# Optimization experiments

Measured on AMD Instinct MI355X. Metric: run time of the kernel, lower is better.

The kernel has to match this reference:

```python
import jax, jax.numpy as jnp
import numpy as np

FEATURE_DIM = 1024
HEAD_NUM = 16
HIDDEN_DIM = FEATURE_DIM // HEAD_NUM


def setup_inputs() -> dict:
    key = jax.random.key(0)
    ks = jax.random.split(key, 12)
    B, S, D = 4, 2048, FEATURE_DIM
    s = 1.0 / np.sqrt(D)
    inp = {
        "query": jax.random.normal(ks[0], (B, S, D), jnp.float32),
        "key": jax.random.normal(ks[1], (B, S, D), jnp.float32),
        "value": jax.random.normal(ks[2], (B, S, D), jnp.float32),
        "mask": jax.random.randint(ks[3], (B, 1, 1, S), 0, 2, jnp.int32),
        "Wq": jax.random.normal(ks[4], (D, D), jnp.float32) * s,
        "bq": jnp.zeros((D,), jnp.float32),
        "Wk": jax.random.normal(ks[5], (D, D), jnp.float32) * s,
        "bk": jnp.zeros((D,), jnp.float32),
        "Wv": jax.random.normal(ks[6], (D, D), jnp.float32) * s,
        "bv": jnp.zeros((D,), jnp.float32),
        "Wo": jax.random.normal(ks[7], (D, D), jnp.float32) * s,
        "bo": jnp.zeros((D,), jnp.float32),
    }
    return inp


def reference(query, key, value, mask, Wq, bq, Wk, bk, Wv, bv, Wo, bo):
    B, Sq, D = query.shape
    H, Hd = HEAD_NUM, HIDDEN_DIM
    scale = jnp.sqrt(jnp.asarray(Hd, query.dtype))

    def split_heads(x):
        b, s, _ = x.shape
        return x.reshape(b, s, H, Hd).transpose(0, 2, 1, 3)  # [B,H,S,Hd]

    Q = split_heads(query @ Wq.T + bq)
    K = split_heads(key @ Wk.T + bk)
    V = split_heads(value @ Wv.T + bv)

    scores = jnp.einsum("bhqd,bhkd->bhqk", Q, K) / scale
    scores = jnp.where(mask == 0, jnp.asarray(-1e10, scores.dtype), scores)
    attn = jax.nn.softmax(scores, axis=-1)  # dropout p=0 -> identity
    h = jnp.einsum("bhqk,bhkd->bhqd", attn, V)
    h = h.transpose(0, 2, 1, 3).reshape(B, Sq, D)
    return h @ Wo.T + bo
```

## Files before the change

### kernel.cpp

```cpp
#include <hip/hip_runtime.h>
#include <hip/hip_bf16.h>
#include <cstdint>
#include <cstddef>

#define D_MODEL 1024
#define SEQ     2048
#define BATCH   4
#define NHEAD   16
#define HD      64
#define MROWS   (BATCH * SEQ)

typedef __attribute__((ext_vector_type(8))) short  short8;
typedef __attribute__((ext_vector_type(4))) float  floatx4;
typedef __attribute__((ext_vector_type(4))) unsigned short ushort4v;
typedef unsigned short u16;

__device__ __forceinline__ u16 f2bf(float x) {
    __hip_bfloat16 h = __float2bfloat16(x);
    return *(u16*)&h;
}

__device__ __forceinline__ void async_copy16(const u16* g, u16* l) {
    __builtin_amdgcn_global_load_lds(
        (const __attribute__((address_space(1))) void*)g,
        (__attribute__((address_space(3))) void*)l, 16, 0, 0);
}

__device__ __forceinline__ void cvt8(const float* s, u16* d, size_t i) {
    const float4 a = *(const float4*)(s + i);
    const float4 b = *(const float4*)(s + i + 4);
    short8 o;
    o[0] = (short)f2bf(a.x); o[1] = (short)f2bf(a.y);
    o[2] = (short)f2bf(a.z); o[3] = (short)f2bf(a.w);
    o[4] = (short)f2bf(b.x); o[5] = (short)f2bf(b.y);
    o[6] = (short)f2bf(b.z); o[7] = (short)f2bf(b.w);
    *(short8*)(d + i) = o;
}

__global__ __launch_bounds__(256) void cvt4(
    const float* __restrict__ s0, const float* __restrict__ s1,
    const float* __restrict__ s2, const float* __restrict__ s3,
    u16* __restrict__ d0, u16* __restrict__ d1,
    u16* __restrict__ d2, u16* __restrict__ d3)
{
    const float* s = blockIdx.y == 0 ? s0 : (blockIdx.y == 1 ? s1 :
                     (blockIdx.y == 2 ? s2 : s3));
    u16*         d = blockIdx.y == 0 ? d0 : (blockIdx.y == 1 ? d1 :
                     (blockIdx.y == 2 ? d2 : d3));
    cvt8(s, d, ((size_t)blockIdx.x * 256 + threadIdx.x) * 8);
}

__global__ __launch_bounds__(256) void gemm_qkv(
    const float* __restrict__ Aq, const float* __restrict__ Ak,
    const float* __restrict__ Av,
    const u16* __restrict__ Wqp, const u16* __restrict__ Wkp,
    const u16* __restrict__ Wvp,
    const float* __restrict__ bqp, const float* __restrict__ bkp,
    const float* __restrict__ bvp,
    u16* __restrict__ oq, u16* __restrict__ ok, u16* __restrict__ ov)
{
    constexpr int K = D_MODEL;
    __shared__ __align__(16) u16 smem[16384];
    u16 (*As)[64] = (u16(*)[64])smem;
    u16 (*Ws)[64] = (u16(*)[64])(smem + 8192);

    const int z = blockIdx.z;
    const float* A    = z == 0 ? Aq  : (z == 1 ? Ak  : Av);
    const u16*   W    = z == 0 ? Wqp : (z == 1 ? Wkp : Wvp);
    const float* bias = z == 0 ? bqp : (z == 1 ? bkp : bvp);
    u16*         out  = z == 0 ? oq  : (z == 1 ? ok  : ov);

    const int bm = blockIdx.x * 128;
    const int bn = blockIdx.y * 128;
    const int t  = threadIdx.x;
    const int w  = t >> 6;
    const int l  = t & 63;
    const int li = l & 15;
    const int quad = l >> 4;
    const int wm = (w & 1) * 64;
    const int wn = (w >> 1) * 64;
    const int srow = w * 32 + (l >> 3);
    const int lc8  = (l & 7) * 8;

    const float* Ab = A + (size_t)bm * K;
    const u16*   Wb = W + (size_t)bn * K;

    float4 pa[4][2];
    short8 pw[4];
    #pragma unroll
    for (int j = 0; j < 4; j++) {
        const float* ap = Ab + (size_t)(srow + j * 8) * K + lc8;
        pa[j][0] = *(const float4*)ap;
        pa[j][1] = *(const float4*)(ap + 4);
        pw[j] = *(const short8*)(Wb + (size_t)(srow + j * 8) * K + lc8);
    }

    floatx4 acc[4][4];
    #pragma unroll
    for (int mi = 0; mi < 4; mi++)
        #pragma unroll
        for (int ni = 0; ni < 4; ni++) acc[mi][ni] = (floatx4){0.f,0.f,0.f,0.f};

    for (int kt = 0; kt < K; kt += 64) {
        __syncthreads();
        #pragma unroll
        for (int j = 0; j < 4; j++) {
            short8 av;
            av[0] = (short)f2bf(pa[j][0].x); av[1] = (short)f2bf(pa[j][0].y);
            av[2] = (short)f2bf(pa[j][0].z); av[3] = (short)f2bf(pa[j][0].w);
            av[4] = (short)f2bf(pa[j][1].x); av[5] = (short)f2bf(pa[j][1].y);
            av[6] = (short)f2bf(pa[j][1].z); av[7] = (short)f2bf(pa[j][1].w);
            *(short8*)&As[srow + j * 8][lc8] = av;
            *(short8*)&Ws[srow + j * 8][lc8] = pw[j];
        }
        __syncthreads();
        if (kt + 64 < K) {
            #pragma unroll
            for (int j = 0; j < 4; j++) {
                const float* ap = Ab + (size_t)(srow + j * 8) * K + kt + 64 + lc8;
                pa[j][0] = *(const float4*)ap;
                pa[j][1] = *(const float4*)(ap + 4);
                pw[j] = *(const short8*)(Wb + (size_t)(srow + j * 8) * K + kt + 64 + lc8);
            }
        }
        #pragma unroll
        for (int ks = 0; ks < 2; ks++) {
            short8 af[4], bf[4];
            #pragma unroll
            for (int i = 0; i < 4; i++) {
                af[i] = *(const short8*)&As[wm + i * 16 + li][ks * 32 + quad * 8];
                bf[i] = *(const short8*)&Ws[wn + i * 16 + li][ks * 32 + quad * 8];
            }
            #pragma unroll
            for (int mi = 0; mi < 4; mi++)
                #pragma unroll
                for (int ni = 0; ni < 4; ni++)
                    acc[mi][ni] = __builtin_amdgcn_mfma_f32_16x16x32_bf16(
                        af[mi], bf[ni], acc[mi][ni], 0, 0, 0);
        }
    }

    if (z < 2) {
        #pragma unroll
        for (int mi = 0; mi < 4; mi++)
            #pragma unroll
            for (int ni = 0; ni < 4; ni++) {
                const int c  = bn + wn + ni * 16 + li;
                const int h  = c >> 6;
                const int hd = c & 63;
                const float bz = bias[c];
                #pragma unroll
                for (int reg = 0; reg < 4; reg++) {
                    const int r = bm + wm + mi * 16 + quad * 4 + reg;
                    const int b = r >> 11;
                    const int s = r & (SEQ - 1);
                    out[(((size_t)(b * NHEAD + h) * SEQ) + s) * HD + hd] = f2bf(acc[mi][ni][reg] + bz);
                }
            }
    } else {
        u16 (*Ct)[128] = (u16(*)[128])smem;
        __syncthreads();
        #pragma unroll
        for (int mi = 0; mi < 4; mi++)
            #pragma unroll
            for (int ni = 0; ni < 4; ni++) {
                const int cl = wn + ni * 16 + li;
                const float bz = bias[bn + cl];
                #pragma unroll
                for (int reg = 0; reg < 4; reg++) {
                    const int rl = wm + mi * 16 + quad * 4 + reg;
                    Ct[cl][rl] = f2bf(acc[mi][ni][reg] + bz);
                }
            }
        __syncthreads();
        const int cl   = t >> 1;
        const int half = t & 1;
        const int cg = bn + cl;
        const int h  = cg >> 6;
        const int hd = cg & 63;
        const int b  = bm >> 11;
        const int s0 = (bm & (SEQ - 1)) + half * 64;
        u16* dst = out + (((size_t)(b * NHEAD + h) * HD) + hd) * SEQ + s0;
        const short8* sp = (const short8*)&Ct[cl][half * 64];
        #pragma unroll
        for (int i = 0; i < 8; i++) ((short8*)dst)[i] = sp[i];
    }
}

__global__ __launch_bounds__(256) void gemm_out(
    const u16* __restrict__ A,
    const u16* __restrict__ W,
    const float* __restrict__ bias,
    float* __restrict__ out)
{
    constexpr int K = D_MODEL;
    __shared__ __align__(16) u16 smem[16384];
    u16 (*As)[64] = (u16(*)[64])smem;
    u16 (*Ws)[64] = (u16(*)[64])(smem + 8192);

    const int bm = blockIdx.x * 128;
    const int bn = blockIdx.y * 128;
    const int t  = threadIdx.x;
    const int w  = t >> 6;
    const int l  = t & 63;
    const int li = l & 15;
    const int quad = l >> 4;
    const int wm = (w & 1) * 64;
    const int wn = (w >> 1) * 64;
    const int lrow = l >> 3;
    const int lcol = (l & 7) * 8;

    const u16* Ag = A + (size_t)bm * K;
    const u16* Wg = W + (size_t)bn * K;

    floatx4 acc[4][4];
    #pragma unroll
    for (int mi = 0; mi < 4; mi++)
        #pragma unroll
        for (int ni = 0; ni < 4; ni++) acc[mi][ni] = (floatx4){0.f,0.f,0.f,0.f};

    for (int kt = 0; kt < K; kt += 64) {
        __syncthreads();
        #pragma unroll
        for (int j = 0; j < 4; j++) {
            const int r = w * 32 + j * 8;
            async_copy16(Ag + (size_t)(r + lrow) * K + kt + lcol, &As[r][0]);
            async_copy16(Wg + (size_t)(r + lrow) * K + kt + lcol, &Ws[r][0]);
        }
        __syncthreads();

        #pragma unroll
        for (int ks = 0; ks < 2; ks++) {
            short8 af[4], bf[4];
            #pragma unroll
            for (int i = 0; i < 4; i++) {
                af[i] = *(const short8*)&As[wm + i * 16 + li][ks * 32 + quad * 8];
                bf[i] = *(const short8*)&Ws[wn + i * 16 + li][ks * 32 + quad * 8];
            }
            #pragma unroll
            for (int mi = 0; mi < 4; mi++)
                #pragma unroll
                for (int ni = 0; ni < 4; ni++)
                    acc[mi][ni] = __builtin_amdgcn_mfma_f32_16x16x32_bf16(
                        af[mi], bf[ni], acc[mi][ni], 0, 0, 0);
        }
    }

    #pragma unroll
    for (int mi = 0; mi < 4; mi++)
        #pragma unroll
        for (int ni = 0; ni < 4; ni++) {
            const int c = bn + wn + ni * 16 + li;
            const float bz = bias[c];
            #pragma unroll
            for (int reg = 0; reg < 4; reg++) {
                const int r = bm + wm + mi * 16 + quad * 4 + reg;
                out[(size_t)r * D_MODEL + c] = acc[mi][ni][reg] + bz;
            }
        }
}

#define LOG2E   1.44269504088896340736f
#define CSCALE  (0.125f * LOG2E)

__global__ __launch_bounds__(256) void attn_mfma(
    const u16* __restrict__ Q,
    const u16* __restrict__ K,
    const u16* __restrict__ Vt,
    const int* __restrict__ mask,
    u16* __restrict__ H)
{
    __shared__ __align__(16) u16 Ks[64 * 64];
    __shared__ __align__(16) u16 Vs[64 * 64];
    __shared__ __align__(16) u16 Ps[4][32][72];
    __shared__ __align__(16) float mc[64];

    const int bh  = blockIdx.y;
    const int b   = bh >> 4;
    const int h   = bh & 15;
    const int q0  = blockIdx.x * 128;
    const int t   = threadIdx.x;
    const int w   = t >> 6;
    const int l   = t & 63;
    const int li  = l & 15;
    const int quad  = l >> 4;
    const int lrow8 = l >> 3;
    const int gch   = (l & 7) ^ lrow8;
    const int swz   = li & 7;

    short8 qf[2][2];
    #pragma unroll
    for (int qb = 0; qb < 2; qb++) {
        const u16* Qrow = Q + ((size_t)bh * SEQ + q0 + w * 32 + qb * 16 + li) * HD;
        qf[qb][0] = *(const short8*)(Qrow + quad * 8);
        qf[qb][1] = *(const short8*)(Qrow + 32 + quad * 8);
    }

    const u16* Kbh = K  + (size_t)bh * SEQ * HD;
    const u16* Vbh = Vt + (size_t)bh * HD * SEQ;
    const int* mg  = mask + (size_t)b * SEQ;

    floatx4 oacc[4][2];
    #pragma unroll
    for (int hm = 0; hm < 4; hm++)
        #pragma unroll
        for (int qb = 0; qb < 2; qb++) oacc[hm][qb] = (floatx4){0.f,0.f,0.f,0.f};
    float rs[2] = {0.f, 0.f};

    #pragma unroll
    for (int j = 0; j < 2; j++) {
        const int rb = w * 16 + j * 8;
        async_copy16(Kbh + (size_t)(rb + lrow8) * HD + gch * 8, &Ks[rb * 64]);
    }
    if (t < 64) mc[t] = (mg[t] != 0) ? -16.0f : -1.0e9f;

    for (int kt = 0; kt < SEQ; kt += 64) {
        __syncthreads();

        #pragma unroll
        for (int j = 0; j < 2; j++) {
            const int rb = w * 16 + j * 8;
            async_copy16(Vbh + (size_t)(rb + lrow8) * SEQ + kt + gch * 8,
                         &Vs[rb * 64]);
        }

        floatx4 sacc[4][2];
        #pragma unroll
        for (int kb = 0; kb < 4; kb++)
            #pragma unroll
            for (int qb = 0; qb < 2; qb++) sacc[kb][qb] = (floatx4){0.f,0.f,0.f,0.f};
        #pragma unroll
        for (int ks = 0; ks < 2; ks++) {
            short8 kf[4];
            #pragma unroll
            for (int kb = 0; kb < 4; kb++)
                kf[kb] = *(const short8*)&Ks[(kb * 16 + li) * 64 + ((ks * 4 + quad) ^ swz) * 8];
            __builtin_amdgcn_s_setprio(1);
            #pragma unroll
            for (int kb = 0; kb < 4; kb++)
                #pragma unroll
                for (int qb = 0; qb < 2; qb++)
                    sacc[kb][qb] = __builtin_amdgcn_mfma_f32_16x16x32_bf16(
                        kf[kb], qf[qb][ks], sacc[kb][qb], 0, 0, 0);
            __builtin_amdgcn_s_setprio(0);
        }

        #pragma unroll
        for (int kb = 0; kb < 4; kb++) {
            const float4 m4 = *(const float4*)&mc[kb * 16 + quad * 4];
            #pragma unroll
            for (int qb = 0; qb < 2; qb++) {
                const float p0 = __builtin_amdgcn_exp2f(fmaf(sacc[kb][qb][0], CSCALE, m4.x));
                const float p1 = __builtin_amdgcn_exp2f(fmaf(sacc[kb][qb][1], CSCALE, m4.y));
                const float p2 = __builtin_amdgcn_exp2f(fmaf(sacc[kb][qb][2], CSCALE, m4.z));
                const float p3 = __builtin_amdgcn_exp2f(fmaf(sacc[kb][qb][3], CSCALE, m4.w));
                rs[qb] += (p0 + p1) + (p2 + p3);
                ushort4v pk;
                pk[0] = f2bf(p0); pk[1] = f2bf(p1);
                pk[2] = f2bf(p2); pk[3] = f2bf(p3);
                *(ushort4v*)&Ps[w][qb * 16 + li][kb * 16 + quad * 4] = pk;
            }
        }

        __syncthreads();

        if (kt + 64 < SEQ) {
            #pragma unroll
            for (int j = 0; j < 2; j++) {
                const int rb = w * 16 + j * 8;
                async_copy16(Kbh + (size_t)(kt + 64 + rb + lrow8) * HD + gch * 8,
                             &Ks[rb * 64]);
            }
            if (t < 64) mc[t] = (mg[kt + 64 + t] != 0) ? -16.0f : -1.0e9f;
        }

        #pragma unroll
        for (int ks = 0; ks < 2; ks++) {
            short8 pf[2];
            #pragma unroll
            for (int qb = 0; qb < 2; qb++)
                pf[qb] = *(const short8*)&Ps[w][qb * 16 + li][ks * 32 + quad * 8];
            __builtin_amdgcn_s_setprio(1);
            #pragma unroll
            for (int hm = 0; hm < 4; hm++) {
                const short8 vf = *(const short8*)&Vs[(hm * 16 + li) * 64 + ((ks * 4 + quad) ^ swz) * 8];
                #pragma unroll
                for (int qb = 0; qb < 2; qb++)
                    oacc[hm][qb] = __builtin_amdgcn_mfma_f32_16x16x32_bf16(
                        vf, pf[qb], oacc[hm][qb], 0, 0, 0);
            }
            __builtin_amdgcn_s_setprio(0);
        }
    }

    float linv[2];
    #pragma unroll
    for (int qb = 0; qb < 2; qb++) {
        float v = rs[qb];
        v += __shfl_xor(v, 16, 64);
        v += __shfl_xor(v, 32, 64);
        linv[qb] = 1.0f / v;
    }
    #pragma unroll
    for (int qb = 0; qb < 2; qb++) {
        const size_t row = (size_t)b * SEQ + q0 + w * 32 + qb * 16 + li;
        #pragma unroll
        for (int hm = 0; hm < 4; hm++) {
            ushort4v o;
            #pragma unroll
            for (int reg = 0; reg < 4; reg++)
                o[reg] = f2bf(oacc[hm][qb][reg] * linv[qb]);
            *(ushort4v*)&H[row * D_MODEL + h * 64 + hm * 16 + quad * 4] = o;
        }
    }
}

extern "C" void kernel_launch(void* const* d_in, const int* in_sizes, int n_in,
                              void* d_out, int out_size, void* d_ws, size_t ws_size,
                              hipStream_t stream)
{
    const float* query = (const float*)d_in[0];
    const float* key_  = (const float*)d_in[1];
    const float* value = (const float*)d_in[2];
    const int*   mask  = (const int*)  d_in[3];
    const float* Wq = (const float*)d_in[4];
    const float* bq = (const float*)d_in[5];
    const float* Wk = (const float*)d_in[6];
    const float* bk = (const float*)d_in[7];
    const float* Wv = (const float*)d_in[8];
    const float* bv = (const float*)d_in[9];
    const float* Wo = (const float*)d_in[10];
    const float* bo = (const float*)d_in[11];
    float* out = (float*)d_out;

    const size_t per = (size_t)BATCH * NHEAD * SEQ * HD;
    const size_t wsz = (size_t)D_MODEL * D_MODEL;
    u16* Qb  = (u16*)d_ws;
    u16* Kb  = Qb  + per;
    u16* Vtb = Kb  + per;
    u16* Hb  = Vtb + per;
    u16* Wqb = Hb  + per;
    u16* Wkb = Wqb + wsz;
    u16* Wvb = Wkb + wsz;
    u16* Wob = Wvb + wsz;

    cvt4<<<dim3(wsz / 2048, 4), 256, 0, stream>>>(Wq, Wk, Wv, Wo,
                                                  Wqb, Wkb, Wvb, Wob);

    gemm_qkv<<<dim3(MROWS / 128, D_MODEL / 128, 3), 256, 0, stream>>>(
        query, key_, value, Wqb, Wkb, Wvb, bq, bk, bv, Qb, Kb, Vtb);

    attn_mfma<<<dim3(SEQ / 128, BATCH * NHEAD), 256, 0, stream>>>(
        Qb, Kb, Vtb, mask, Hb);

    gemm_out<<<dim3(MROWS / 128, D_MODEL / 128), 256, 0, stream>>>(
        Hb, Wob, bo, out);
}
```

Measured before the change: 371.1 us.

## Pre-convert activations to bf16 and use async global-to-LDS loads in QKV GEMM

The conversion kernel now also turns query, key and value into bf16 buffers, one grid row per tensor, with a bounds check so the shorter weight rows stop early. gemm_qkv then reads bf16 activations and fills its LDS tiles with global_load_lds direct copies, replacing the fp32 register prefetch and the in-loop conversion. The aim is to halve the GEMM's repeated A-tile traffic and remove conversion ALU work from the GEMM's inner loop. The cost is an extra full pass over the activations and the loss of register double-buffering, so global latency is no longer hidden behind the MFMA work. The head-output buffer now reuses the converted-query buffer, which is safe because attention runs only after gemm_qkv finishes.

```diff
diff --git a/kernel.cpp b/kernel.cpp
--- a/kernel.cpp
+++ b/kernel.cpp
@@ -37,22 +37,36 @@
     *(short8*)(d + i) = o;
 }
 
-__global__ __launch_bounds__(256) void cvt4(
+__global__ __launch_bounds__(256) void cvt7(
     const float* __restrict__ s0, const float* __restrict__ s1,
     const float* __restrict__ s2, const float* __restrict__ s3,
+    const float* __restrict__ s4, const float* __restrict__ s5,
+    const float* __restrict__ s6,
     u16* __restrict__ d0, u16* __restrict__ d1,
-    u16* __restrict__ d2, u16* __restrict__ d3)
+    u16* __restrict__ d2, u16* __restrict__ d3,
+    u16* __restrict__ d4, u16* __restrict__ d5,
+    u16* __restrict__ d6)
 {
-    const float* s = blockIdx.y == 0 ? s0 : (blockIdx.y == 1 ? s1 :
-                     (blockIdx.y == 2 ? s2 : s3));
-    u16*         d = blockIdx.y == 0 ? d0 : (blockIdx.y == 1 ? d1 :
-                     (blockIdx.y == 2 ? d2 : d3));
-    cvt8(s, d, ((size_t)blockIdx.x * 256 + threadIdx.x) * 8);
+    const int y = blockIdx.y;
+    const float* s;
+    u16* d;
+    size_t n;
+    switch (y) {
+        case 0: s = s0; d = d0; n = (size_t)D_MODEL * D_MODEL; break;
+        case 1: s = s1; d = d1; n = (size_t)D_MODEL * D_MODEL; break;
+        case 2: s = s2; d = d2; n = (size_t)D_MODEL * D_MODEL; break;
+        case 3: s = s3; d = d3; n = (size_t)D_MODEL * D_MODEL; break;
+        case 4: s = s4; d = d4; n = (size_t)MROWS * D_MODEL;   break;
+        case 5: s = s5; d = d5; n = (size_t)MROWS * D_MODEL;   break;
+        default: s = s6; d = d6; n = (size_t)MROWS * D_MODEL;  break;
+    }
+    const size_t i = ((size_t)blockIdx.x * 256 + threadIdx.x) * 8;
+    if (i < n) cvt8(s, d, i);
 }
 
 __global__ __launch_bounds__(256) void gemm_qkv(
-    const float* __restrict__ Aq, const float* __restrict__ Ak,
-    const float* __restrict__ Av,
+    const u16* __restrict__ Aq, const u16* __restrict__ Ak,
+    const u16* __restrict__ Av,
     const u16* __restrict__ Wqp, const u16* __restrict__ Wkp,
     const u16* __restrict__ Wvp,
     const float* __restrict__ bqp, const float* __restrict__ bkp,
@@ -65,7 +79,7 @@
     u16 (*Ws)[64] = (u16(*)[64])(smem + 8192);
 
     const int z = blockIdx.z;
-    const float* A    = z == 0 ? Aq  : (z == 1 ? Ak  : Av);
+    const u16*   A    = z == 0 ? Aq  : (z == 1 ? Ak  : Av);
     const u16*   W    = z == 0 ? Wqp : (z == 1 ? Wkp : Wvp);
     const float* bias = z == 0 ? bqp : (z == 1 ? bkp : bvp);
     u16*         out  = z == 0 ? oq  : (z == 1 ? ok  : ov);
@@ -79,21 +93,11 @@
     const int quad = l >> 4;
     const int wm = (w & 1) * 64;
     const int wn = (w >> 1) * 64;
-    const int srow = w * 32 + (l >> 3);
-    const int lc8  = (l & 7) * 8;
-
-    const float* Ab = A + (size_t)bm * K;
-    const u16*   Wb = W + (size_t)bn * K;
-
-    float4 pa[4][2];
-    short8 pw[4];
-    #pragma unroll
-    for (int j = 0; j < 4; j++) {
-        const float* ap = Ab + (size_t)(srow + j * 8) * K + lc8;
-        pa[j][0] = *(const float4*)ap;
-        pa[j][1] = *(const float4*)(ap + 4);
-        pw[j] = *(const short8*)(Wb + (size_t)(srow + j * 8) * K + lc8);
-    }
+    const int lrow = l >> 3;
+    const int lcol = (l & 7) * 8;
+
+    const u16* Ag = A + (size_t)bm * K;
+    const u16* Wg = W + (size_t)bn * K;
 
     floatx4 acc[4][4];
     #pragma unroll
@@ -105,24 +109,12 @@
         __syncthreads();
         #pragma unroll
         for (int j = 0; j < 4; j++) {
-            short8 av;
-            av[0] = (short)f2bf(pa[j][0].x); av[1] = (short)f2bf(pa[j][0].y);
-            av[2] = (short)f2bf(pa[j][0].z); av[3] = (short)f2bf(pa[j][0].w);
-            av[4] = (short)f2bf(pa[j][1].x); av[5] = (short)f2bf(pa[j][1].y);
-            av[6] = (short)f2bf(pa[j][1].z); av[7] = (short)f2bf(pa[j][1].w);
-            *(short8*)&As[srow + j * 8][lc8] = av;
-            *(short8*)&Ws[srow + j * 8][lc8] = pw[j];
-        }
-        __syncthreads();
-        if (kt + 64 < K) {
-            #pragma unroll
-            for (int j = 0; j < 4; j++) {
-                const float* ap = Ab + (size_t)(srow + j * 8) * K + kt + 64 + lc8;
-                pa[j][0] = *(const float4*)ap;
-                pa[j][1] = *(const float4*)(ap + 4);
-                pw[j] = *(const short8*)(Wb + (size_t)(srow + j * 8) * K + kt + 64 + lc8);
-            }
-        }
+            const int r = w * 32 + j * 8;
+            async_copy16(Ag + (size_t)(r + lrow) * K + kt + lcol, &As[r][0]);
+            async_copy16(Wg + (size_t)(r + lrow) * K + kt + lcol, &Ws[r][0]);
+        }
+        __syncthreads();
+
         #pragma unroll
         for (int ks = 0; ks < 2; ks++) {
             short8 af[4], bf[4];
@@ -438,17 +430,21 @@
     u16* Qb  = (u16*)d_ws;
     u16* Kb  = Qb  + per;
     u16* Vtb = Kb  + per;
-    u16* Hb  = Vtb + per;
-    u16* Wqb = Hb  + per;
+    u16* Wqb = Vtb + per;
     u16* Wkb = Wqb + wsz;
     u16* Wvb = Wkb + wsz;
     u16* Wob = Wvb + wsz;
-
-    cvt4<<<dim3(wsz / 2048, 4), 256, 0, stream>>>(Wq, Wk, Wv, Wo,
-                                                  Wqb, Wkb, Wvb, Wob);
+    u16* Aqb = Wob + wsz;
+    u16* Akb = Aqb + per;
+    u16* Avb = Akb + per;
+    u16* Hb  = Aqb;
+
+    cvt7<<<dim3((per / 8 + 255) / 256, 7), 256, 0, stream>>>(
+        Wq, Wk, Wv, Wo, query, key_, value,
+        Wqb, Wkb, Wvb, Wob, Aqb, Akb, Avb);
 
     gemm_qkv<<<dim3(MROWS / 128, D_MODEL / 128, 3), 256, 0, stream>>>(
-        query, key_, value, Wqb, Wkb, Wvb, bq, bk, bv, Qb, Kb, Vtb);
+        Aqb, Akb, Avb, Wqb, Wkb, Wvb, bq, bk, bv, Qb, Kb, Vtb);
 
     attn_mfma<<<dim3(SEQ / 128, BATCH * NHEAD), 256, 0, stream>>>(
         Qb, Kb, Vtb, mask, Hb);
```

New measurement: 374.2 us. No clear change (+0.8%).
